# Kernel optimization log

Hardware: AMD Instinct MI355X
Metric: run time of the kernel (lower is better)

## Reference

```python
import jax, jax.numpy as jnp
import numpy as np

GRID = 4096
WINDOW_SIZES = (128, 256, 512)  # self.window_schedule in the torch module
BLOCK_FRAC = 0.2                # fraction of blocked (fixed) cells


def setup_inputs() -> dict:
    key = jax.random.key(0)
    u = jax.random.uniform(key, (GRID, GRID), dtype=jnp.float32)
    # blocked cells > 0.0, free cells == 0.0 (binary fixed-cell occupancy mask)
    mask = (u > (1.0 - BLOCK_FRAC)).astype(jnp.float32)
    # the torch code requires the grid center (or an 8-neighbor) to be free;
    # force it free so the seed location is static.
    mask = mask.at[GRID // 2, GRID // 2].set(0.0)
    return {"fixed_cell_mask": mask}


def _dilate4(r):
    # 4-connected dilation of a boolean map (matches BFS neighbor set)
    up = jnp.pad(r[1:, :], ((0, 1), (0, 0)))
    dn = jnp.pad(r[:-1, :], ((1, 0), (0, 0)))
    lf = jnp.pad(r[:, 1:], ((0, 0), (0, 1)))
    rt = jnp.pad(r[:, :-1], ((0, 0), (1, 0)))
    return r | up | dn | lf | rt


def _flood_fill(free, cx, cy):
    """Parallel label-propagation equivalent of the serial BFS flood fill:
    reachable set of `free` cells 4-connected to seed (cx, cy). The seed is
    always tagged, exactly as in get_contiguous_free_region_in_window."""
    seed = jnp.zeros(free.shape, dtype=bool).at[cx, cy].set(True)

    def cond(state):
        reach, prev_count = state
        return jnp.sum(reach) != prev_count

    def body(state):
        reach, _ = state
        new = (_dilate4(reach) & free) | seed
        return new, jnp.sum(reach)

    reach, _ = jax.lax.while_loop(cond, body, (seed, jnp.int32(-1)))
    return reach


def reference(fixed_cell_mask):
    """Faithful JAX version of assemble_free_region_masks: for each window
    size, extract the centered window, flood-fill the contiguous free region
    from the center, and scatter it back into a full-grid boolean mask.
    Returns (masks [len(WINDOW_SIZES), H, W] float32, counts [len] int32)."""
    H, W = fixed_cell_mask.shape
    cx, cy = H // 2, W // 2  # seed is free by construction (see setup_inputs)
    masks, counts = [], []
    for size in WINDOW_SIZES:
        half = size // 2
        sx, ex = max(0, cx - half), min(H, cx + half)
        sy, ey = max(0, cy - half), min(W, cy + half)
        window = fixed_cell_mask[sx:ex, sy:ey]
        free = window == 0.0
        reach = _flood_fill(free, cx - sx, cy - sy)
        full = jnp.zeros((H, W), dtype=bool).at[sx:ex, sy:ey].set(reach)
        masks.append(full)
        counts.append(jnp.sum(reach))
    return jnp.stack(masks).astype(jnp.float32), jnp.stack(counts).astype(jnp.int32)
```

## Files before the change

kernel.cpp:

```cpp
#include <hip/hip_runtime.h>
#include <stdint.h>

#define GRID_N 4096
#define CELL_BLOCKS 1344
#define TILE_BLOCKS 336
#define EDGE_BLOCKS 77
#define ZERO_BLOCKS 8192

typedef float vfloat4 __attribute__((ext_vector_type(4)));

__device__ inline void decode_block(int b, int& w, int& S, int& lg, int& off,
                                    int& woff, int& baseblk) {
    if (b < 64)       { w = 0; S = 128; lg = 7; off = 1984; woff = 0;     baseblk = 0;   }
    else if (b < 320) { w = 1; S = 256; lg = 8; off = 1920; woff = 16384; baseblk = 64;  }
    else              { w = 2; S = 512; lg = 9; off = 1792; woff = 81920; baseblk = 320; }
}

__device__ inline void decode_tile(int b, int& S, int& lg, int& off, int& woff,
                                   int& tileR, int& tileC) {
    int t, tsh;
    if (b < 16)      { S = 128; lg = 7; off = 1984; woff = 0;     t = b;      tsh = 2; }
    else if (b < 80) { S = 256; lg = 8; off = 1920; woff = 16384; t = b - 16; tsh = 3; }
    else             { S = 512; lg = 9; off = 1792; woff = 81920; t = b - 80; tsh = 4; }
    tileR = t >> tsh;
    tileC = t & ((1 << tsh) - 1);
}

__device__ inline int uf_find(int* L, int a) {
    int p = __hip_atomic_load(&L[a], __ATOMIC_RELAXED, __HIP_MEMORY_SCOPE_AGENT);
    while (p != a) {
        a = p;
        p = __hip_atomic_load(&L[a], __ATOMIC_RELAXED, __HIP_MEMORY_SCOPE_AGENT);
    }
    return a;
}
__device__ inline void uf_union(int* L, int a, int b) {
    while (true) {
        a = uf_find(L, a);
        b = uf_find(L, b);
        if (a == b) return;
        if (a < b) { int t = a; a = b; b = t; }
        int old = atomicMin(&L[a], b);
        if (old == a) return;
        a = old;
    }
}

__device__ inline int lfind(int* lab, int a) {
    int p = __hip_atomic_load(&lab[a], __ATOMIC_RELAXED, __HIP_MEMORY_SCOPE_WORKGROUP);
    while (p != a) {
        a = p;
        p = __hip_atomic_load(&lab[a], __ATOMIC_RELAXED, __HIP_MEMORY_SCOPE_WORKGROUP);
    }
    return a;
}
__device__ inline void lunion(int* lab, int a, int b) {
    while (true) {
        a = lfind(lab, a);
        b = lfind(lab, b);
        if (a == b) return;
        if (a < b) { int t = a; a = b; b = t; }
        int old = atomicMin(&lab[a], b);
        if (old == a) return;
        a = old;
    }
}

__global__ void k_local(const float* __restrict__ mask, int* __restrict__ L) {
    int S, lg, off, woff, tileR, tileC;
    decode_tile(blockIdx.x, S, lg, off, woff, tileR, tileC);
    __shared__ int lab[1024];

    #pragma unroll
    for (int k = 0; k < 4; k++) {
        int l = threadIdx.x + k * 256;
        int lr = l >> 5, lc = l & 31;
        int gr = tileR * 32 + lr, gc = tileC * 32 + lc;
        size_t g = (size_t)(off + gr) * GRID_N + (size_t)(off + gc);
        lab[l] = (mask[g] == 0.0f) ? l : -1;
    }
    __syncthreads();

    #pragma unroll
    for (int k = 0; k < 4; k++) {
        int l = threadIdx.x + k * 256;
        if (lab[l] == -1) continue;
        int lr = l >> 5, lc = l & 31;
        if (lc + 1 < 32 && lab[l + 1] != -1)  lunion(lab, l, l + 1);
        if (lr + 1 < 32 && lab[l + 32] != -1) lunion(lab, l, l + 32);
    }
    __syncthreads();

    #pragma unroll
    for (int k = 0; k < 4; k++) {
        int l = threadIdx.x + k * 256;
        int lr = l >> 5, lc = l & 31;
        int gidx = (tileR * 32 + lr) * S + tileC * 32 + lc;
        if (lab[l] == -1) {
            L[woff + gidx] = -1;
        } else {
            int r = lfind(lab, l);
            int rr = r >> 5, rc = r & 31;
            L[woff + gidx] = (tileR * 32 + rr) * S + tileC * 32 + rc;
        }
    }
}

__global__ void k_zero_merge(int* __restrict__ L, float* __restrict__ out,
                             int out_size) {
    int b = blockIdx.x;
    if (b < EDGE_BLOCKS) {
        int e = b * 256 + threadIdx.x;
        int S, lg, woff, i; bool horiz;
        if (e < 768)        { S = 128; lg = 7; woff = 0;     horiz = e < 384;   i = horiz ? e : e - 384; }
        else if (e < 4352)  { S = 256; lg = 8; woff = 16384; horiz = e < 2560;  i = horiz ? e - 768 : e - 2560; }
        else                { S = 512; lg = 9; woff = 81920; horiz = e < 12032; i = horiz ? e - 4352 : e - 12032; }
        int bi = i >> lg;
        int* Lw = L + woff;
        int a, n;
        if (horiz) { int r = i & (S - 1); int c = bi * 32 + 31; a = r * S + c; n = a + 1; }
        else       { int c = i & (S - 1); int r = bi * 32 + 31; a = r * S + c; n = a + S; }
        if (Lw[a] != -1 && Lw[n] != -1) uf_union(Lw, a, n);
    } else {
        long long n4 = (long long)(out_size >> 2);
        long long i = (long long)(b - EDGE_BLOCKS) * 256 + threadIdx.x;
        long long stride = (long long)(gridDim.x - EDGE_BLOCKS) * 256;
        vfloat4* o4 = (vfloat4*)out;
        vfloat4 z = (vfloat4)(0.0f);
        for (; i < n4; i += stride) __builtin_nontemporal_store(z, &o4[i]);
        long long t = (long long)(b - EDGE_BLOCKS) * 256 + threadIdx.x;
        long long tail = (long long)out_size - n4 * 4;
        if (t < tail) out[n4 * 4 + t] = 0.0f;
    }
}

__global__ void k_write(int* __restrict__ L, float* __restrict__ out) {
    int b = blockIdx.x;
    int w, S, lg, off, woff, baseblk;
    decode_block(b, w, S, lg, off, woff, baseblk);
    int idx = (b - baseblk) * 256 + threadIdx.x;
    int* Lw = L + woff;

    __shared__ int rootC;
    __shared__ float wsum[4];
    if (threadIdx.x == 0) {
        int centerIdx = (S >> 1) * S + (S >> 1);
        rootC = uf_find(Lw, centerIdx);
    }
    __syncthreads();

    int lab = Lw[idx];
    bool reach = false;
    if (lab != -1) {
        int root = uf_find(Lw, idx);
        Lw[idx] = root;
        reach = (root == rootC);
    }
    int r = idx >> lg;
    int c = idx & (S - 1);
    size_t go = (size_t)w * GRID_N * GRID_N + (size_t)(off + r) * GRID_N + (size_t)(off + c);
    out[go] = reach ? 1.0f : 0.0f;

    unsigned long long m = __ballot(reach);
    int lane = threadIdx.x & 63;
    int wv = threadIdx.x >> 6;
    if (lane == 0) wsum[wv] = (float)__popcll(m);
    __syncthreads();
    if (threadIdx.x == 0) {
        float s = wsum[0] + wsum[1] + wsum[2] + wsum[3];
        atomicAdd(&out[(size_t)3 * GRID_N * GRID_N + w], s);
    }
}

extern "C" void kernel_launch(void* const* d_in, const int* in_sizes, int n_in,
                              void* d_out, int out_size, void* d_ws, size_t ws_size,
                              hipStream_t stream) {
    const float* mask = (const float*)d_in[0];
    float* out = (float*)d_out;
    int* L = (int*)d_ws;

    k_local<<<TILE_BLOCKS, 256, 0, stream>>>(mask, L);
    k_zero_merge<<<EDGE_BLOCKS + ZERO_BLOCKS, 256, 0, stream>>>(L, out, out_size);
    k_write<<<CELL_BLOCKS, 256, 0, stream>>>(L, out);
}
```

Baseline: 274.0 us.

## Fuse tile labeling with output zeroing and merge edges in a single block

The per-tile local labeling now runs in the same launch as the output zeroing, so the two overlap. Tile-edge unions move into a separate one-block kernel of 1024 threads that walks all edges and then flattens the labels of edge cells. The global find now uses path halving with compare-exchange. This trades a fully parallel edge-merge grid for a serial-ish single block, which could become a bottleneck, but it should keep the later per-cell find chains short.

```diff
diff --git a/kernel.cpp b/kernel.cpp
--- a/kernel.cpp
+++ b/kernel.cpp
@@ -4,7 +4,7 @@
 #define GRID_N 4096
 #define CELL_BLOCKS 1344
 #define TILE_BLOCKS 336
-#define EDGE_BLOCKS 77
+#define NUM_EDGES 19712
 #define ZERO_BLOCKS 8192
 
 typedef float vfloat4 __attribute__((ext_vector_type(4)));
@@ -27,12 +27,15 @@
 }
 
 __device__ inline int uf_find(int* L, int a) {
-    int p = __hip_atomic_load(&L[a], __ATOMIC_RELAXED, __HIP_MEMORY_SCOPE_AGENT);
-    while (p != a) {
-        a = p;
-        p = __hip_atomic_load(&L[a], __ATOMIC_RELAXED, __HIP_MEMORY_SCOPE_AGENT);
+    while (true) {
+        int p = __hip_atomic_load(&L[a], __ATOMIC_RELAXED, __HIP_MEMORY_SCOPE_AGENT);
+        if (p == a) return a;
+        int gp = __hip_atomic_load(&L[p], __ATOMIC_RELAXED, __HIP_MEMORY_SCOPE_AGENT);
+        if (gp == p) return p;
+        __hip_atomic_compare_exchange_strong(&L[a], &p, gp,
+            __ATOMIC_RELAXED, __ATOMIC_RELAXED, __HIP_MEMORY_SCOPE_AGENT);
+        a = gp;
     }
-    return a;
 }
 __device__ inline void uf_union(int* L, int a, int b) {
     while (true) {
@@ -66,71 +69,83 @@
     }
 }
 
-__global__ void k_local(const float* __restrict__ mask, int* __restrict__ L) {
-    int S, lg, off, woff, tileR, tileC;
-    decode_tile(blockIdx.x, S, lg, off, woff, tileR, tileC);
-    __shared__ int lab[1024];
+__global__ void k_init_zero(const float* __restrict__ mask, int* __restrict__ L,
+                            float* __restrict__ out, int out_size) {
+    int b = blockIdx.x;
+    if (b < TILE_BLOCKS) {
+        int S, lg, off, woff, tileR, tileC;
+        decode_tile(b, S, lg, off, woff, tileR, tileC);
+        __shared__ int lab[1024];
 
-    #pragma unroll
-    for (int k = 0; k < 4; k++) {
-        int l = threadIdx.x + k * 256;
-        int lr = l >> 5, lc = l & 31;
-        int gr = tileR * 32 + lr, gc = tileC * 32 + lc;
-        size_t g = (size_t)(off + gr) * GRID_N + (size_t)(off + gc);
-        lab[l] = (mask[g] == 0.0f) ? l : -1;
-    }
-    __syncthreads();
+        #pragma unroll
+        for (int k = 0; k < 4; k++) {
+            int l = threadIdx.x + k * 256;
+            int lr = l >> 5, lc = l & 31;
+            size_t g = (size_t)(off + tileR * 32 + lr) * GRID_N
+                     + (size_t)(off + tileC * 32 + lc);
+            lab[l] = (mask[g] == 0.0f) ? l : -1;
+        }
+        __syncthreads();
 
-    #pragma unroll
-    for (int k = 0; k < 4; k++) {
-        int l = threadIdx.x + k * 256;
-        if (lab[l] == -1) continue;
-        int lr = l >> 5, lc = l & 31;
-        if (lc + 1 < 32 && lab[l + 1] != -1)  lunion(lab, l, l + 1);
-        if (lr + 1 < 32 && lab[l + 32] != -1) lunion(lab, l, l + 32);
-    }
-    __syncthreads();
+        #pragma unroll
+        for (int k = 0; k < 4; k++) {
+            int l = threadIdx.x + k * 256;
+            if (lab[l] == -1) continue;
+            int lr = l >> 5, lc = l & 31;
+            if (lc + 1 < 32 && lab[l + 1] != -1)  lunion(lab, l, l + 1);
+            if (lr + 1 < 32 && lab[l + 32] != -1) lunion(lab, l, l + 32);
+        }
+        __syncthreads();
 
-    #pragma unroll
-    for (int k = 0; k < 4; k++) {
-        int l = threadIdx.x + k * 256;
-        int lr = l >> 5, lc = l & 31;
-        int gidx = (tileR * 32 + lr) * S + tileC * 32 + lc;
-        if (lab[l] == -1) {
-            L[woff + gidx] = -1;
-        } else {
-            int r = lfind(lab, l);
-            int rr = r >> 5, rc = r & 31;
-            L[woff + gidx] = (tileR * 32 + rr) * S + tileC * 32 + rc;
+        #pragma unroll
+        for (int k = 0; k < 4; k++) {
+            int l = threadIdx.x + k * 256;
+            int lr = l >> 5, lc = l & 31;
+            int gidx = (tileR * 32 + lr) * S + tileC * 32 + lc;
+            if (lab[l] == -1) {
+                L[woff + gidx] = -1;
+            } else {
+                int r = lfind(lab, l);
+                int rr = r >> 5, rc = r & 31;
+                L[woff + gidx] = (tileR * 32 + rr) * S + tileC * 32 + rc;
+            }
         }
+    } else {
+        long long n4 = (long long)(out_size >> 2);
+        long long i = (long long)(b - TILE_BLOCKS) * 256 + threadIdx.x;
+        long long stride = (long long)ZERO_BLOCKS * 256;
+        vfloat4* o4 = (vfloat4*)out;
+        vfloat4 z = (vfloat4)(0.0f);
+        for (; i < n4; i += stride) __builtin_nontemporal_store(z, &o4[i]);
+        long long t = (long long)(b - TILE_BLOCKS) * 256 + threadIdx.x;
+        long long tail = (long long)out_size - n4 * 4;
+        if (t < tail) out[n4 * 4 + t] = 0.0f;
     }
 }
 
-__global__ void k_zero_merge(int* __restrict__ L, float* __restrict__ out,
-                             int out_size) {
-    int b = blockIdx.x;
-    if (b < EDGE_BLOCKS) {
-        int e = b * 256 + threadIdx.x;
-        int S, lg, woff, i; bool horiz;
-        if (e < 768)        { S = 128; lg = 7; woff = 0;     horiz = e < 384;   i = horiz ? e : e - 384; }
-        else if (e < 4352)  { S = 256; lg = 8; woff = 16384; horiz = e < 2560;  i = horiz ? e - 768 : e - 2560; }
-        else                { S = 512; lg = 9; woff = 81920; horiz = e < 12032; i = horiz ? e - 4352 : e - 12032; }
-        int bi = i >> lg;
-        int* Lw = L + woff;
-        int a, n;
-        if (horiz) { int r = i & (S - 1); int c = bi * 32 + 31; a = r * S + c; n = a + 1; }
-        else       { int c = i & (S - 1); int r = bi * 32 + 31; a = r * S + c; n = a + S; }
+__device__ inline void decode_edge(int e, int*& Lw, int& a, int& n, int* L) {
+    int S, lg, woff, i; bool horiz;
+    if (e < 768)        { S = 128; lg = 7; woff = 0;     horiz = e < 384;   i = horiz ? e : e - 384; }
+    else if (e < 4352)  { S = 256; lg = 8; woff = 16384; horiz = e < 2560;  i = horiz ? e - 768 : e - 2560; }
+    else                { S = 512; lg = 9; woff = 81920; horiz = e < 12032; i = horiz ? e - 4352 : e - 12032; }
+    int bi = i >> lg;
+    Lw = L + woff;
+    if (horiz) { int r = i & (S - 1); int c = bi * 32 + 31; a = r * S + c; n = a + 1; }
+    else       { int c = i & (S - 1); int r = bi * 32 + 31; a = r * S + c; n = a + S; }
+}
+
+__global__ void k_merge(int* __restrict__ L) {
+    for (int e = threadIdx.x; e < NUM_EDGES; e += blockDim.x) {
+        int *Lw, a, n;
+        decode_edge(e, Lw, a, n, L);
         if (Lw[a] != -1 && Lw[n] != -1) uf_union(Lw, a, n);
-    } else {
-        long long n4 = (long long)(out_size >> 2);
-        long long i = (long long)(b - EDGE_BLOCKS) * 256 + threadIdx.x;
-        long long stride = (long long)(gridDim.x - EDGE_BLOCKS) * 256;
-        vfloat4* o4 = (vfloat4*)out;
-        vfloat4 z = (vfloat4)(0.0f);
-        for (; i < n4; i += stride) __builtin_nontemporal_store(z, &o4[i]);
-        long long t = (long long)(b - EDGE_BLOCKS) * 256 + threadIdx.x;
-        long long tail = (long long)out_size - n4 * 4;
-        if (t < tail) out[n4 * 4 + t] = 0.0f;
+    }
+    __syncthreads();
+    for (int e = threadIdx.x; e < NUM_EDGES; e += blockDim.x) {
+        int *Lw, a, n;
+        decode_edge(e, Lw, a, n, L);
+        if (Lw[a] != -1) { int r = uf_find(Lw, a); Lw[a] = r; }
+        if (Lw[n] != -1) { int r = uf_find(Lw, n); Lw[n] = r; }
     }
 }
 
@@ -153,7 +168,6 @@
     bool reach = false;
     if (lab != -1) {
         int root = uf_find(Lw, idx);
-        Lw[idx] = root;
         reach = (root == rootC);
     }
     int r = idx >> lg;
@@ -179,7 +193,7 @@
     float* out = (float*)d_out;
     int* L = (int*)d_ws;
 
-    k_local<<<TILE_BLOCKS, 256, 0, stream>>>(mask, L);
-    k_zero_merge<<<EDGE_BLOCKS + ZERO_BLOCKS, 256, 0, stream>>>(L, out, out_size);
+    k_init_zero<<<TILE_BLOCKS + ZERO_BLOCKS, 256, 0, stream>>>(mask, L, out, out_size);
+    k_merge<<<1, 1024, 0, stream>>>(L);
     k_write<<<CELL_BLOCKS, 256, 0, stream>>>(L, out);
 }
```

Result: slower. 556.9 us (+103.3%).
